# Optimization experiments

Measured on AMD Instinct MI355X. Metric: run time of the kernel, lower is better.

Reference implementation:

```python
import jax, jax.numpy as jnp
import numpy as np

B, C, H, W, D = 2, 256, 16, 16, 16
HEADS, DIM_HEAD = 8, 64
HIDDEN = HEADS * DIM_HEAD  # 512
EPS = 1e-12  # torch F.normalize default eps


def setup_inputs() -> dict:
    key = jax.random.key(0)
    k1, k2, k3 = jax.random.split(key, 3)
    x = jax.random.normal(k1, (B, C, H, W, D), dtype=jnp.float32)
    g = jnp.ones((C,), dtype=jnp.float32)
    # conv 1x1 weights act as plain matrices over the channel dim
    w_qkv = jax.random.normal(k2, (3 * HIDDEN, C), dtype=jnp.float32) * (C ** -0.5)
    w_out = jax.random.normal(k3, (C, HIDDEN), dtype=jnp.float32) * (HIDDEN ** -0.5)
    b_out = jnp.zeros((C,), dtype=jnp.float32)
    return {"x": x, "g": g, "w_qkv": w_qkv, "w_out": w_out, "b_out": b_out}


def reference(x, g, w_qkv, w_out, b_out):
    b, c, h, w, d = x.shape
    n = h * w * d
    # RMSNorm3D: F.normalize(x, dim=1) * g * sqrt(C)
    norm = jnp.sqrt(jnp.sum(x * x, axis=1, keepdims=True))
    xn = x / jnp.maximum(norm, EPS) * g[None, :, None, None, None] * (c ** 0.5)
    xt = xn.reshape(b, c, n)  # [b, c, n]
    # 1x1 conv3d == channel matmul
    qkv = jnp.einsum('oc,bcn->bon', w_qkv, xt)  # [b, 3*hidden, n]
    q, k, v = jnp.split(qkv, 3, axis=1)
    def to_heads(t):  # [b, heads*dh, n] -> [b, heads, n, dh]
        return t.reshape(b, HEADS, DIM_HEAD, n).transpose(0, 1, 3, 2)
    q, k, v = to_heads(q), to_heads(k), to_heads(v)
    scale = DIM_HEAD ** -0.5
    sim = jnp.einsum('bhid,bhjd->bhij', q * scale, k)  # [b, heads, n, n]
    attn = jax.nn.softmax(sim, axis=-1)
    out = jnp.einsum('bhij,bhjd->bhid', attn, v)  # [b, heads, n, dh]
    out = out.transpose(0, 1, 3, 2).reshape(b, HIDDEN, n)  # [b, hidden, n]
    y = jnp.einsum('oc,bcn->bon', w_out, out) + b_out[None, :, None]
    return y.reshape(b, c, h, w, d)
```

## Files before the change

### kernel.cpp

```cpp
#include <hip/hip_runtime.h>
#include <type_traits>

#define DI __device__ __forceinline__

typedef __attribute__((ext_vector_type(8))) __bf16 vbf8;
typedef __attribute__((ext_vector_type(8))) short  vs8;
typedef __attribute__((ext_vector_type(4))) float  f4;
typedef __attribute__((ext_vector_type(4))) unsigned int u32x4;

static constexpr int BB   = 2;
static constexpr int C    = 256;
static constexpr int NN   = 4096;
static constexpr int HID  = 512;
static constexpr int QKVR = 1536;

static DI unsigned short f2bf(float f) {
  unsigned int u = __builtin_bit_cast(unsigned int, f);
  u += 0x7fffu + ((u >> 16) & 1u);
  return (unsigned short)(u >> 16);
}
static DI float bf2f(unsigned short u) {
  return __builtin_bit_cast(float, (unsigned int)u << 16);
}
static DI unsigned int cvtpk(float lo, float hi) {
  unsigned int r;
  asm("v_cvt_pk_bf16_f32 %0, %1, %2" : "=v"(r) : "v"(lo), "v"(hi));
  return r;
}
static DI float EXP2(float x) {
  float r;
  asm("v_exp_f32 %0, %1" : "=v"(r) : "v"(x));
  return r;
}

template <typename V>
static DI auto mfma_sel(V a, V b, f4 c, int)
    -> decltype(__builtin_amdgcn_mfma_f32_16x16x32_bf16(a, b, c, 0, 0, 0)) {
  return __builtin_amdgcn_mfma_f32_16x16x32_bf16(a, b, c, 0, 0, 0);
}
template <typename V>
static DI f4 mfma_sel(V a, V b, f4 c, long) {
  return __builtin_amdgcn_mfma_f32_16x16x32_bf16(
      __builtin_bit_cast(vs8, a), __builtin_bit_cast(vs8, b), c, 0, 0, 0);
}
static DI f4 MFMA(vs8 a, vs8 b, f4 c) {
  return mfma_sel(__builtin_bit_cast(vbf8, a), __builtin_bit_cast(vbf8, b), c, 0);
}

static DI void gll16(const unsigned short* g, unsigned short* l) {
  __builtin_amdgcn_global_load_lds(
      (const __attribute__((address_space(1))) unsigned int*)g,
      (__attribute__((address_space(3))) unsigned int*)l, 16, 0, 0);
}

__global__ void k_prep(const float* __restrict__ wqkv, const float* __restrict__ g,
                       const float* __restrict__ wout,
                       unsigned short* __restrict__ wg, unsigned short* __restrict__ wo) {
  int i = blockIdx.x * 256 + threadIdx.x;
  if (i < QKVR * C) wg[i] = f2bf(wqkv[i] * g[i & (C - 1)]);
  if (i < C * HID)  wo[i] = f2bf(wout[i]);
}

__global__ __launch_bounds__(256) void k_qkv(const float* __restrict__ x,
    const unsigned short* __restrict__ wg,
    unsigned short* __restrict__ qo, unsigned short* __restrict__ ko,
    unsigned short* __restrict__ vo) {
  __shared__ unsigned short xs[64 * 264];
  __shared__ float ps[4][64];
  __shared__ float inv[64];
  const int bo = blockIdx.x % 6;
  const int bn = (blockIdx.x / 6) & 63;
  const int b  = blockIdx.x / 384;
  const int o0 = bo * 256, n0 = bn * 64;
  const int tid = threadIdx.x;
  {
    const int nl = tid & 63, cb = tid >> 6;
    const float* xp = x + (size_t)b * C * NN + n0 + nl;
    float s = 0.f;
    #pragma unroll
    for (int k8 = 0; k8 < 8; ++k8) {
      float v[8];
      #pragma unroll
      for (int j = 0; j < 8; ++j) {
        v[j] = xp[(size_t)(cb * 64 + k8 * 8 + j) * NN];
        s += v[j] * v[j];
      }
      u32x4 pk;
      pk[0] = cvtpk(v[0], v[1]); pk[1] = cvtpk(v[2], v[3]);
      pk[2] = cvtpk(v[4], v[5]); pk[3] = cvtpk(v[6], v[7]);
      *(u32x4*)(&xs[nl * 264 + cb * 64 + k8 * 8]) = pk;
    }
    ps[cb][nl] = s;
  }
  __syncthreads();
  if (tid < 64) {
    float t4 = ps[0][tid] + ps[1][tid] + ps[2][tid] + ps[3][tid];
    inv[tid] = 16.0f / fmaxf(sqrtf(t4), 1e-12f);
  }
  __syncthreads();
  const int wave = tid >> 6, lane = tid & 63, lr = lane & 15, lg = lane >> 4;
  const int orow = o0 + wave * 64;
  f4 acc[4][4];
  #pragma unroll
  for (int om = 0; om < 4; ++om)
    #pragma unroll
    for (int nc = 0; nc < 4; ++nc) acc[om][nc] = f4{0.f, 0.f, 0.f, 0.f};
  const unsigned short* wpb = wg + (size_t)(orow + lr) * C + lg * 8;
  #pragma unroll
  for (int c0 = 0; c0 < C; c0 += 32) {
    vs8 bfv[4];
    #pragma unroll
    for (int nc = 0; nc < 4; ++nc)
      bfv[nc] = *(const vs8*)(&xs[(nc * 16 + lr) * 264 + c0 + lg * 8]);
    #pragma unroll
    for (int om = 0; om < 4; ++om) {
      vs8 af = *(const vs8*)(wpb + (size_t)om * 16 * C + c0);
      #pragma unroll
      for (int nc = 0; nc < 4; ++nc) acc[om][nc] = MFMA(af, bfv[nc], acc[om][nc]);
    }
  }
  #pragma unroll
  for (int om = 0; om < 4; ++om) {
    const int om_row = orow + om * 16;
    const int otype = om_row >> 9;
    const int head  = (om_row >> 6) & 7;
    const int bh    = b * 8 + head;
    const int dbase = (om_row & 63) + lg * 4;
    #pragma unroll
    for (int nc = 0; nc < 4; ++nc) {
      const int n = n0 + nc * 16 + lr;
      float s = inv[nc * 16 + lr];
      if (otype == 0) s *= 0.125f * 1.44269504088896f;
      if (otype < 2) {
        unsigned short* dst = (otype == 0 ? qo : ko) + ((size_t)bh * NN + n) * 64 + dbase;
        unsigned long long pk = 0;
        #pragma unroll
        for (int r = 0; r < 4; ++r)
          pk |= (unsigned long long)f2bf(acc[om][nc][r] * s) << (16 * r);
        *(unsigned long long*)dst = pk;
      } else {
        const int np = n0 + ((nc >> 1) << 5) + ((lr >> 2) << 3) + ((nc & 1) << 2) + (lr & 3);
        #pragma unroll
        for (int r = 0; r < 4; ++r)
          vo[((size_t)bh * 64 + dbase + r) * NN + np] = f2bf(acc[om][nc][r] * s);
      }
    }
  }
}

template <int SPLITS>
__global__ __launch_bounds__(256, 4) void k_attn(const unsigned short* __restrict__ qq,
    const unsigned short* __restrict__ kk, const unsigned short* __restrict__ vv,
    unsigned short* __restrict__ ou, float* __restrict__ st) {
  __shared__ unsigned short stg[2][8192];
  constexpr int NB  = 512 * SPLITS;
  constexpr int CPX = NB / 8;
  constexpr int JCH = NN / SPLITS / 64;
  const int bid = blockIdx.x;
  const int swz = (bid & 7) * CPX + (bid >> 3);
  const int qt   = swz & 31;
  const int rest = swz >> 5;
  const int sp   = (SPLITS > 1) ? (rest % SPLITS) : 0;
  const int bh   = (SPLITS > 1) ? (rest / SPLITS) : rest;
  const int js   = sp * (NN / SPLITS);
  const int tid = threadIdx.x, wave = tid >> 6, lane = tid & 63;
  const int lr = lane & 15, lg = lane >> 4;
  const int qbase = qt * 128 + wave * 32;
  const unsigned short* kb = kk + (size_t)bh * NN * 64;
  const unsigned short* vb = vv + (size_t)bh * 64 * NN;
  vs8 qf[2][2];
  #pragma unroll
  for (int qn = 0; qn < 2; ++qn)
    #pragma unroll
    for (int kd = 0; kd < 2; ++kd)
      qf[qn][kd] = *(const vs8*)(qq + ((size_t)bh * NN + qbase + qn * 16 + lr) * 64 + kd * 32 + lg * 8);
  const vs8 onesf = {0x3F80, 0x3F80, 0x3F80, 0x3F80, 0x3F80, 0x3F80, 0x3F80, 0x3F80};
  const f4 zero4 = {0.f, 0.f, 0.f, 0.f};
  f4 oacc[4][2] = { { {0,0,0,0},{0,0,0,0} }, { {0,0,0,0},{0,0,0,0} },
                    { {0,0,0,0},{0,0,0,0} }, { {0,0,0,0},{0,0,0,0} } };
  f4 lacc[2] = { {0,0,0,0}, {0,0,0,0} };

  auto stage = [&](int j0, int buf) {
    #pragma unroll
    for (int p = 0; p < 2; ++p) {
      const int g  = wave * 2 + p;
      const int jt = g >> 1, kd = g & 1;
      gll16(kb + (size_t)(j0 + jt * 16 + lr) * 64 + kd * 32 + lg * 8,
            &stg[buf][g * 512]);
      const int dt = g >> 1, kj = g & 1;
      gll16(vb + (size_t)(dt * 16 + lr) * NN + j0 + kj * 32 + lg * 8,
            &stg[buf][4096 + g * 512]);
    }
  };

  stage(js, 0);
  asm volatile("s_waitcnt vmcnt(0)");
  __syncthreads();

  for (int t = 0; t < JCH; ++t) {
    const int cur = t & 1;
    if (t + 1 < JCH) stage(js + (t + 1) * 64, cur ^ 1);
    const unsigned short* sbk = stg[cur];
    const unsigned short* sbv = stg[cur] + 4096;
    f4 s[4][2];
    __builtin_amdgcn_s_setprio(1);
    #pragma unroll
    for (int jt = 0; jt < 4; ++jt) {
      vs8 k0 = *(const vs8*)(sbk + (jt * 2 + 0) * 512 + lane * 8);
      vs8 k1 = *(const vs8*)(sbk + (jt * 2 + 1) * 512 + lane * 8);
      #pragma unroll
      for (int qn = 0; qn < 2; ++qn) {
        s[jt][qn] = MFMA(k0, qf[qn][0], zero4);
        s[jt][qn] = MFMA(k1, qf[qn][1], s[jt][qn]);
      }
    }
    __builtin_amdgcn_s_setprio(0);
    vs8 pb[2][2];
    #pragma unroll
    for (int qn = 0; qn < 2; ++qn)
      #pragma unroll
      for (int kj = 0; kj < 2; ++kj) {
        u32x4 w;
        w[0] = cvtpk(EXP2(s[2 * kj][qn][0]),     EXP2(s[2 * kj][qn][1]));
        w[1] = cvtpk(EXP2(s[2 * kj][qn][2]),     EXP2(s[2 * kj][qn][3]));
        w[2] = cvtpk(EXP2(s[2 * kj + 1][qn][0]), EXP2(s[2 * kj + 1][qn][1]));
        w[3] = cvtpk(EXP2(s[2 * kj + 1][qn][2]), EXP2(s[2 * kj + 1][qn][3]));
        pb[qn][kj] = __builtin_bit_cast(vs8, w);
      }
    __builtin_amdgcn_s_setprio(1);
    #pragma unroll
    for (int kj = 0; kj < 2; ++kj) {
      #pragma unroll
      for (int mt = 0; mt < 4; ++mt) {
        vs8 vf = *(const vs8*)(sbv + (mt * 2 + kj) * 512 + lane * 8);
        oacc[mt][0] = MFMA(vf, pb[0][kj], oacc[mt][0]);
        oacc[mt][1] = MFMA(vf, pb[1][kj], oacc[mt][1]);
      }
      lacc[0] = MFMA(onesf, pb[0][kj], lacc[0]);
      lacc[1] = MFMA(onesf, pb[1][kj], lacc[1]);
    }
    __builtin_amdgcn_s_setprio(0);
    asm volatile("s_waitcnt vmcnt(0)");
    __syncthreads();
  }
  const int b = bh >> 3, h = bh & 7;
  float rl2[2] = {1.f, 1.f};
  if (SPLITS == 1) { rl2[0] = 1.0f / lacc[0][0]; rl2[1] = 1.0f / lacc[1][0]; }
  const size_t rowbase = (size_t)((SPLITS > 1 ? sp * BB : 0) + b) * NN;
  #pragma unroll
  for (int mt = 0; mt < 4; ++mt)
    #pragma unroll
    for (int qn = 0; qn < 2; ++qn) {
      unsigned int w0 = cvtpk(oacc[mt][qn][0] * rl2[qn], oacc[mt][qn][1] * rl2[qn]);
      unsigned int w1 = cvtpk(oacc[mt][qn][2] * rl2[qn], oacc[mt][qn][3] * rl2[qn]);
      const int q = qbase + qn * 16 + lr;
      *(unsigned long long*)(&ou[(rowbase + q) * HID + h * 64 + mt * 16 + lg * 4]) =
          ((unsigned long long)w1 << 32) | w0;
    }
  if (SPLITS > 1 && lg == 0) {
    #pragma unroll
    for (int qn = 0; qn < 2; ++qn)
      st[(size_t)(sp * 16 + bh) * NN + qbase + qn * 16 + lr] = lacc[qn][0];
  }
}

template <int SPLITS>
__global__ __launch_bounds__(256) void k_out(const unsigned short* __restrict__ ou,
    const float* __restrict__ st, const unsigned short* __restrict__ wo,
    const float* __restrict__ bout, float* __restrict__ y) {
  __shared__ unsigned short os[64 * 136];
  const int bo = blockIdx.x & 3;
  const int bn = (blockIdx.x >> 2) & 63;
  const int b  = blockIdx.x >> 8;
  const int o0 = bo * 64, n0 = bn * 64;
  const int tid = threadIdx.x, wave = tid >> 6, lane = tid & 63, lr = lane & 15, lg = lane >> 4;
  const int orow = o0 + wave * 16;
  f4 acc[4] = { {0,0,0,0},{0,0,0,0},{0,0,0,0},{0,0,0,0} };
  for (int c0 = 0; c0 < HID; c0 += 128) {
    __syncthreads();
    {
      const int nl = tid & 63, cb = tid >> 6;
      const int n = n0 + nl;
      if (SPLITS == 1) {
        const unsigned short* sp0 = ou + ((size_t)b * NN + n) * HID + c0 + cb * 32;
        #pragma unroll
        for (int t = 0; t < 4; ++t)
          *(u32x4*)(&os[nl * 136 + cb * 32 + t * 8]) = *(const u32x4*)(sp0 + t * 8);
      } else {
        const int h  = (c0 + cb * 32) >> 6;
        const int bh = b * 8 + h;
        float lsum = 0.f;
        #pragma unroll
        for (int s = 0; s < SPLITS; ++s) lsum += st[(size_t)(s * 16 + bh) * NN + n];
        const float rl = 1.0f / lsum;
        #pragma unroll
        for (int t = 0; t < 4; ++t) {
          const int cc = cb * 32 + t * 8;
          float a[8] = {0,0,0,0,0,0,0,0};
          #pragma unroll
          for (int s = 0; s < SPLITS; ++s) {
            vs8 v = *(const vs8*)(&ou[((size_t)(s * BB + b) * NN + n) * HID + c0 + cc]);
            #pragma unroll
            for (int j = 0; j < 8; ++j) a[j] += bf2f((unsigned short)v[j]);
          }
          u32x4 pk;
          pk[0] = cvtpk(a[0] * rl, a[1] * rl);
          pk[1] = cvtpk(a[2] * rl, a[3] * rl);
          pk[2] = cvtpk(a[4] * rl, a[5] * rl);
          pk[3] = cvtpk(a[6] * rl, a[7] * rl);
          *(u32x4*)(&os[nl * 136 + cc]) = pk;
        }
      }
    }
    __syncthreads();
    const unsigned short* wp = wo + (size_t)(orow + lr) * HID + c0 + lg * 8;
    #pragma unroll
    for (int cc0 = 0; cc0 < 128; cc0 += 32) {
      vs8 af = *(const vs8*)(wp + cc0);
      #pragma unroll
      for (int nc = 0; nc < 4; ++nc) {
        vs8 bf = *(const vs8*)(&os[(nc * 16 + lr) * 136 + cc0 + lg * 8]);
        acc[nc] = MFMA(af, bf, acc[nc]);
      }
    }
  }
  #pragma unroll
  for (int nc = 0; nc < 4; ++nc) {
    const int n = n0 + nc * 16 + lr;
    #pragma unroll
    for (int r = 0; r < 4; ++r)
      y[((size_t)b * C + orow + lg * 4 + r) * NN + n] = acc[nc][r] + bout[orow + lg * 4 + r];
  }
}

extern "C" void kernel_launch(void* const* d_in, const int* in_sizes, int n_in,
                              void* d_out, int out_size, void* d_ws, size_t ws_size,
                              hipStream_t stream) {
  const float* x    = (const float*)d_in[0];
  const float* g    = (const float*)d_in[1];
  const float* wqkv = (const float*)d_in[2];
  const float* wout = (const float*)d_in[3];
  const float* bout = (const float*)d_in[4];
  float* y = (float*)d_out;
  char* ws = (char*)d_ws;
  unsigned short* wg  = (unsigned short*)(ws);
  unsigned short* wo  = (unsigned short*)(ws + 786432);
  unsigned short* qb  = (unsigned short*)(ws + 1048576);
  unsigned short* kb  = (unsigned short*)(ws + 1048576 + 8388608);
  unsigned short* vtb = (unsigned short*)(ws + 1048576 + 2 * 8388608);
  unsigned short* ou  = (unsigned short*)(ws + 1048576 + 3 * 8388608);
  k_prep<<<1536, 256, 0, stream>>>(wqkv, g, wout, wg, wo);
  k_qkv<<<768, 256, 0, stream>>>(x, wg, qb, kb, vtb);
  const size_t base  = 1048576ull + 3ull * 8388608;
  const size_t stsz  = 16ull * 4096 * 4;
  const size_t need2 = base + 2ull * 8388608 + 2 * stsz;
  if (ws_size >= need2) {
    float* st = (float*)(ws + base + 2ull * 8388608);
    k_attn<2><<<1024, 256, 0, stream>>>(qb, kb, vtb, ou, st);
    k_out<2><<<512, 256, 0, stream>>>(ou, st, wo, bout, y);
  } else {
    k_attn<1><<<512, 256, 0, stream>>>(qb, kb, vtb, ou, nullptr);
    k_out<1><<<512, 256, 0, stream>>>(ou, nullptr, wo, bout, y);
  }
}
```

Baseline: 125.0 us.

## Software-pipeline attention loop: overlap next-chunk QK/exp with current PV, triple-buffer LDS

```diff
diff --git a/kernel.cpp b/kernel.cpp
--- a/kernel.cpp
+++ b/kernel.cpp
@@ -152,7 +152,7 @@
 __global__ __launch_bounds__(256, 4) void k_attn(const unsigned short* __restrict__ qq,
     const unsigned short* __restrict__ kk, const unsigned short* __restrict__ vv,
     unsigned short* __restrict__ ou, float* __restrict__ st) {
-  __shared__ unsigned short stg[2][8192];
+  __shared__ unsigned short stg[3][8192];
   constexpr int NB  = 512 * SPLITS;
   constexpr int CPX = NB / 8;
   constexpr int JCH = NN / SPLITS / 64;
@@ -179,6 +179,7 @@
   f4 oacc[4][2] = { { {0,0,0,0},{0,0,0,0} }, { {0,0,0,0},{0,0,0,0} },
                     { {0,0,0,0},{0,0,0,0} }, { {0,0,0,0},{0,0,0,0} } };
   f4 lacc[2] = { {0,0,0,0}, {0,0,0,0} };
+  vs8 pbA[2][2], pbB[2][2];
 
   auto stage = [&](int j0, int buf) {
     #pragma unroll
@@ -193,56 +194,88 @@
     }
   };
 
+#define QKSM(PB, BN)                                                           \
+  {                                                                            \
+    const unsigned short* sbk_ = stg[BN];                                      \
+    _Pragma("unroll") for (int qn = 0; qn < 2; ++qn) {                         \
+      f4 s0 = MFMA(*(const vs8*)(sbk_ + 0 * 512 + lane * 8), qf[qn][0], zero4);\
+      s0 = MFMA(*(const vs8*)(sbk_ + 1 * 512 + lane * 8), qf[qn][1], s0);      \
+      f4 s1 = MFMA(*(const vs8*)(sbk_ + 2 * 512 + lane * 8), qf[qn][0], zero4);\
+      s1 = MFMA(*(const vs8*)(sbk_ + 3 * 512 + lane * 8), qf[qn][1], s1);      \
+      f4 s2 = MFMA(*(const vs8*)(sbk_ + 4 * 512 + lane * 8), qf[qn][0], zero4);\
+      s2 = MFMA(*(const vs8*)(sbk_ + 5 * 512 + lane * 8), qf[qn][1], s2);      \
+      f4 s3 = MFMA(*(const vs8*)(sbk_ + 6 * 512 + lane * 8), qf[qn][0], zero4);\
+      s3 = MFMA(*(const vs8*)(sbk_ + 7 * 512 + lane * 8), qf[qn][1], s3);      \
+      u32x4 w0, w1;                                                            \
+      w0[0] = cvtpk(EXP2(s0[0]), EXP2(s0[1]));                                 \
+      w0[1] = cvtpk(EXP2(s0[2]), EXP2(s0[3]));                                 \
+      w0[2] = cvtpk(EXP2(s1[0]), EXP2(s1[1]));                                 \
+      w0[3] = cvtpk(EXP2(s1[2]), EXP2(s1[3]));                                 \
+      w1[0] = cvtpk(EXP2(s2[0]), EXP2(s2[1]));                                 \
+      w1[1] = cvtpk(EXP2(s2[2]), EXP2(s2[3]));                                 \
+      w1[2] = cvtpk(EXP2(s3[0]), EXP2(s3[1]));                                 \
+      w1[3] = cvtpk(EXP2(s3[2]), EXP2(s3[3]));                                 \
+      PB[qn][0] = __builtin_bit_cast(vs8, w0);                                 \
+      PB[qn][1] = __builtin_bit_cast(vs8, w1);                                 \
+    }                                                                          \
+  }
+
+#define PVOP(PB, BC)                                                           \
+  {                                                                            \
+    const unsigned short* sbv_ = stg[BC] + 4096;                               \
+    _Pragma("unroll") for (int kj = 0; kj < 2; ++kj) {                         \
+      _Pragma("unroll") for (int mt = 0; mt < 4; ++mt) {                       \
+        vs8 vf = *(const vs8*)(sbv_ + (mt * 2 + kj) * 512 + lane * 8);         \
+        oacc[mt][0] = MFMA(vf, PB[0][kj], oacc[mt][0]);                        \
+        oacc[mt][1] = MFMA(vf, PB[1][kj], oacc[mt][1]);                        \
+      }                                                                        \
+      lacc[0] = MFMA(onesf, PB[0][kj], lacc[0]);                               \
+      lacc[1] = MFMA(onesf, PB[1][kj], lacc[1]);                               \
+    }                                                                          \
+  }
+
+#define ITER(T, PBC, PBN, BN, BC, BS, DOSTAGE, DOQK)                           \
+  {                                                                            \
+    if (DOSTAGE) stage(js + ((T) + 2) * 64, BS);                               \
+    __builtin_amdgcn_s_setprio(1);                                             \
+    if (DOQK) QKSM(PBN, BN);                                                   \
+    PVOP(PBC, BC);                                                             \
+    __builtin_amdgcn_s_setprio(0);                                             \
+    asm volatile("s_waitcnt vmcnt(0)");                                        \
+    __syncthreads();                                                           \
+  }
+
   stage(js, 0);
+  stage(js + 64, 1);
   asm volatile("s_waitcnt vmcnt(0)");
   __syncthreads();
-
-  for (int t = 0; t < JCH; ++t) {
-    const int cur = t & 1;
-    if (t + 1 < JCH) stage(js + (t + 1) * 64, cur ^ 1);
-    const unsigned short* sbk = stg[cur];
-    const unsigned short* sbv = stg[cur] + 4096;
-    f4 s[4][2];
-    __builtin_amdgcn_s_setprio(1);
-    #pragma unroll
-    for (int jt = 0; jt < 4; ++jt) {
-      vs8 k0 = *(const vs8*)(sbk + (jt * 2 + 0) * 512 + lane * 8);
-      vs8 k1 = *(const vs8*)(sbk + (jt * 2 + 1) * 512 + lane * 8);
-      #pragma unroll
-      for (int qn = 0; qn < 2; ++qn) {
-        s[jt][qn] = MFMA(k0, qf[qn][0], zero4);
-        s[jt][qn] = MFMA(k1, qf[qn][1], s[jt][qn]);
-      }
-    }
-    __builtin_amdgcn_s_setprio(0);
-    vs8 pb[2][2];
-    #pragma unroll
-    for (int qn = 0; qn < 2; ++qn)
-      #pragma unroll
-      for (int kj = 0; kj < 2; ++kj) {
-        u32x4 w;
-        w[0] = cvtpk(EXP2(s[2 * kj][qn][0]),     EXP2(s[2 * kj][qn][1]));
-        w[1] = cvtpk(EXP2(s[2 * kj][qn][2]),     EXP2(s[2 * kj][qn][3]));
-        w[2] = cvtpk(EXP2(s[2 * kj + 1][qn][0]), EXP2(s[2 * kj + 1][qn][1]));
-        w[3] = cvtpk(EXP2(s[2 * kj + 1][qn][2]), EXP2(s[2 * kj + 1][qn][3]));
-        pb[qn][kj] = __builtin_bit_cast(vs8, w);
-      }
-    __builtin_amdgcn_s_setprio(1);
-    #pragma unroll
-    for (int kj = 0; kj < 2; ++kj) {
-      #pragma unroll
-      for (int mt = 0; mt < 4; ++mt) {
-        vs8 vf = *(const vs8*)(sbv + (mt * 2 + kj) * 512 + lane * 8);
-        oacc[mt][0] = MFMA(vf, pb[0][kj], oacc[mt][0]);
-        oacc[mt][1] = MFMA(vf, pb[1][kj], oacc[mt][1]);
-      }
-      lacc[0] = MFMA(onesf, pb[0][kj], lacc[0]);
-      lacc[1] = MFMA(onesf, pb[1][kj], lacc[1]);
-    }
-    __builtin_amdgcn_s_setprio(0);
-    asm volatile("s_waitcnt vmcnt(0)");
-    __syncthreads();
-  }
+  QKSM(pbA, 0);
+
+  constexpr int GROUPS = (JCH - 2) / 6;
+  for (int i = 0; i < GROUPS; ++i) {
+    const int t = i * 6;
+    ITER(t + 0, pbA, pbB, 1, 0, 2, 1, 1);
+    ITER(t + 1, pbB, pbA, 2, 1, 0, 1, 1);
+    ITER(t + 2, pbA, pbB, 0, 2, 1, 1, 1);
+    ITER(t + 3, pbB, pbA, 1, 0, 2, 1, 1);
+    ITER(t + 4, pbA, pbB, 2, 1, 0, 1, 1);
+    ITER(t + 5, pbB, pbA, 0, 2, 1, 1, 1);
+  }
+  constexpr int TB = GROUPS * 6;
+  if constexpr (JCH - TB == 2) {
+    ITER(TB + 0, pbA, pbB, 1, 0, 2, 0, 1);
+    ITER(TB + 1, pbB, pbA, 2, 1, 0, 0, 0);
+  } else {
+    ITER(TB + 0, pbA, pbB, 1, 0, 2, 1, 1);
+    ITER(TB + 1, pbB, pbA, 2, 1, 0, 1, 1);
+    ITER(TB + 2, pbA, pbB, 0, 2, 1, 0, 1);
+    ITER(TB + 3, pbB, pbA, 1, 0, 2, 0, 0);
+  }
+
+#undef ITER
+#undef PVOP
+#undef QKSM
+
   const int b = bh >> 3, h = bh & 7;
   float rl2[2] = {1.f, 1.f};
   if (SPLITS == 1) { rl2[0] = 1.0f / lacc[0][0]; rl2[1] = 1.0f / lacc[1][0]; }
```

Result: no change. 125.0 us (+0.0%).
